# Optimization experiments

Measured on AMD Instinct MI355X. Metric: run time of the kernel, lower is better.

Reference implementation:

```python
import math
import jax, jax.numpy as jnp
import numpy as np

B = 8
NUM_POINTS = 4096
LATENT = 512
HID = 512
AD = 128
R1, R2, R_ATT = 1.0, 1.5, 0.2
EPS = 1e-5
SQRT_D = math.sqrt(AD)


def _fibonacci_sphere_points(n, radius):
    if n <= 0:
        return np.zeros((0, 3), np.float32)
    i = np.arange(n, dtype=np.float32)
    phi = (1 + 5 ** 0.5) / 2
    theta = 2 * math.pi * i / phi
    z = 1.0 - 2.0 * (i + 0.5) / n
    r_xy = np.sqrt(np.maximum(1.0 - z * z, 0.0))
    return (radius * np.stack((r_xy * np.cos(theta), r_xy * np.sin(theta), z), axis=-1)).astype(np.float32)


def _make_template():
    n_shell = NUM_POINTS - 1
    area_ratio = R1 ** 2 / (R1 ** 2 + R2 ** 2)
    n1 = max(1, round(n_shell * area_ratio))
    n2 = n_shell - n1
    if n2 == 0:
        n1, n2 = n1 - 1, 1
    t1 = _fibonacci_sphere_points(n1, R1)
    t2 = _fibonacci_sphere_points(n2, R2)
    return jnp.asarray(np.concatenate([np.zeros((1, 3), np.float32), t1, t2], axis=0))


def setup_inputs() -> dict:
    key = jax.random.key(0)
    ks = iter(jax.random.split(key, 64))
    d = {}
    d['z'] = jax.random.normal(next(ks), (B, LATENT), jnp.float32)
    d['template'] = _make_template()
    d['wq'] = jax.random.normal(next(ks), (AD, 3), jnp.float32) * 0.1
    d['wk'] = jax.random.normal(next(ks), (AD, 3), jnp.float32) * 0.1
    d['wv'] = jax.random.normal(next(ks), (AD, 3), jnp.float32) * 0.1
    in_dims = [LATENT + 3, LATENT + 3 + AD, LATENT + 3 + AD]
    for s, in_dim in enumerate(in_dims):
        d[f's{s}_w1'] = jax.random.normal(next(ks), (HID, in_dim), jnp.float32) * (1.0 / math.sqrt(in_dim))
        d[f's{s}_b1'] = jnp.zeros((HID,), jnp.float32)
        d[f's{s}_g1'] = jnp.ones((HID,), jnp.float32)
        d[f's{s}_be1'] = jnp.zeros((HID,), jnp.float32)
        d[f's{s}_w2'] = jax.random.normal(next(ks), (HID, HID), jnp.float32) * (1.0 / math.sqrt(HID))
        d[f's{s}_b2'] = jnp.zeros((HID,), jnp.float32)
        d[f's{s}_g2'] = jnp.ones((HID,), jnp.float32)
        d[f's{s}_be2'] = jnp.zeros((HID,), jnp.float32)
        d[f's{s}_w3'] = jax.random.normal(next(ks), (3, HID), jnp.float32) * (1.0 / math.sqrt(HID))
        d[f's{s}_b3'] = jnp.zeros((3,), jnp.float32)
    return d


def _bn_relu(x, gamma, beta):
    # BatchNorm1d in training mode over channel dim of (B, N, C): stats over (B, N)
    mean = jnp.mean(x, axis=(0, 1))
    var = jnp.var(x, axis=(0, 1))
    xn = (x - mean) * jax.lax.rsqrt(var + EPS)
    return jax.nn.relu(xn * gamma + beta)


def _stage(x, w1, b1, g1, be1, w2, b2, g2, be2, w3, b3):
    h = _bn_relu(x @ w1.T + b1, g1, be1)
    h = _bn_relu(h @ w2.T + b2, g2, be2)
    return h @ w3.T + b3


def _local_attention(coords, wq, wk, wv):
    Q = coords @ wq.T  # (B, N, AD)
    K = coords @ wk.T
    V = coords @ wv.T
    sq = jnp.sum(coords * coords, axis=-1)  # (B, N)
    D2 = sq[:, :, None] + sq[:, None, :] - 2.0 * jnp.einsum('bnd,bmd->bnm', coords, coords)
    mask = D2 <= R_ATT ** 2  # diagonal always True (D2=0)
    scores = jnp.einsum('bnd,bmd->bnm', Q, K) / SQRT_D
    scores = jnp.where(mask, scores, -jnp.inf)
    W = jax.nn.softmax(scores, axis=-1)
    W = jnp.where(mask, W, 0.0)
    return jnp.einsum('bnm,bmd->bnd', W, V)


def reference(z, template, wq, wk, wv,
              s0_w1, s0_b1, s0_g1, s0_be1, s0_w2, s0_b2, s0_g2, s0_be2, s0_w3, s0_b3,
              s1_w1, s1_b1, s1_g1, s1_be1, s1_w2, s1_b2, s1_g2, s1_be2, s1_w3, s1_b3,
              s2_w1, s2_b1, s2_g1, s2_be1, s2_w2, s2_b2, s2_g2, s2_be2, s2_w3, s2_b3):
    Bz = z.shape[0]
    z_exp = jnp.broadcast_to(z[:, None, :], (Bz, NUM_POINTS, LATENT))
    tmpl = jnp.broadcast_to(template[None], (Bz, NUM_POINTS, 3))
    coords0 = _stage(jnp.concatenate((z_exp, tmpl), axis=-1),
                     s0_w1, s0_b1, s0_g1, s0_be1, s0_w2, s0_b2, s0_g2, s0_be2, s0_w3, s0_b3)
    attn1 = _local_attention(coords0, wq, wk, wv)
    coords1 = _stage(jnp.concatenate((z_exp, coords0, attn1), axis=-1),
                     s1_w1, s1_b1, s1_g1, s1_be1, s1_w2, s1_b2, s1_g2, s1_be2, s1_w3, s1_b3)
    attn2 = _local_attention(coords1, wq, wk, wv)
    coords2 = _stage(jnp.concatenate((z_exp, coords1, attn2), axis=-1),
                     s2_w1, s2_b1, s2_g1, s2_be1, s2_w2, s2_b2, s2_g2, s2_be2, s2_w3, s2_b3)
    return coords2
```

## Files before the change

### kernel.cpp

```cpp
#include <hip/hip_runtime.h>
#include <math.h>

#define NPTS 4096
#define BATCH 8
#define HIDD 512
#define ROWS 32768
#define R_ATT2 0.04f
#define INV_SQRT_D 0.08838834764831845f
#define LOG2E 1.4426950408889634f

typedef unsigned short u16;
typedef unsigned int u32;
typedef __attribute__((ext_vector_type(8))) short s8v;
typedef __attribute__((ext_vector_type(4))) float f4v;
typedef __attribute__((ext_vector_type(4))) u32 u4v;
typedef __attribute__((ext_vector_type(2))) u32 u2v;

__device__ __forceinline__ float u2f(u16 v) { return __uint_as_float(((u32)v) << 16); }
__device__ __forceinline__ u16 f2u(float f) {
  u32 u = __float_as_uint(f);
  return (u16)((u + 0x7fffu + ((u >> 16) & 1u)) >> 16);
}
__device__ __forceinline__ u32 packtrunc(float x0, float x1) {
  return (__float_as_uint(x1) & 0xFFFF0000u) | (__float_as_uint(x0) >> 16);
}
__device__ __forceinline__ float fast_exp2(float x) {
  float r;
  asm("v_exp_f32 %0, %1" : "=v"(r) : "v"(x));
  return r;
}
__device__ __forceinline__ s8v mk8(u32 a, u32 b, u32 c, u32 d) {
  union { u4v u; s8v s; } x;
  x.u = (u4v){a, b, c, d};
  return x.s;
}

__global__ void gram_k(const float* __restrict__ wq, const float* __restrict__ wk,
                       float* __restrict__ G) {
  int ab = threadIdx.x;
  if (ab < 9) {
    int a = ab / 3, b = ab % 3;
    float s = 0.f;
    for (int d = 0; d < 128; ++d) s = fmaf(wq[d * 3 + a], wk[d * 3 + b], s);
    G[ab] = s;
  }
}

__global__ __launch_bounds__(256) void prep2_k(
    const float* __restrict__ z, const float* __restrict__ w1, int ldw,
    const float* __restrict__ b1, const float* __restrict__ w2,
    float* __restrict__ zwbuf, float* __restrict__ ubuf,
    u16* __restrict__ w1abf, u16* __restrict__ w2bf, int doW1a) {
  int wid = blockIdx.x * 4 + (threadIdx.x >> 6);
  int lane = threadIdx.x & 63;
  {
    int b = wid >> 9, c = wid & 511;
    const float* zr = z + b * 512;
    const float* wr = w1 + (size_t)c * ldw;
    float acc = 0.f;
#pragma unroll
    for (int k = lane; k < 512; k += 64) acc = fmaf(zr[k], wr[k], acc);
#pragma unroll
    for (int off = 32; off; off >>= 1) acc += __shfl_down(acc, off);
    if (lane == 0) zwbuf[wid] = acc + b1[c];
  }
  int idx = blockIdx.x * 256 + threadIdx.x;
  if (idx < 1536) {
    int a = idx >> 9, c = idx & 511;
    ubuf[idx] = w1[(size_t)c * ldw + 512 + a];
  }
  if (doW1a && idx < 65536) {
    int n = idx >> 7, k = idx & 127;
    w1abf[idx] = f2u(w1[(size_t)n * 643 + 515 + k]);
  }
  w2bf[idx] = f2u(w2[idx]);
}

__global__ __launch_bounds__(256) void s0l1s_k(const float* __restrict__ tmpl,
                                               const float* __restrict__ u,
                                               const float* __restrict__ zw,
                                               u16* __restrict__ h,
                                               float* __restrict__ psum,
                                               float* __restrict__ psumsq) {
  __shared__ float Ls[4][512];
  __shared__ float Lq[4][512];
  int g = blockIdx.x;
  int wave = threadIdx.x >> 6, lane = threadIdx.x & 63;
  int b = g >> 8;
  int c0 = lane * 8;
  const float* zr = zw + b * 512 + c0;
  const float* u0 = u + c0;
  const float* u1 = u + 512 + c0;
  const float* u2 = u + 1024 + c0;
  float zv[8], u0v[8], u1v[8], u2v[8];
#pragma unroll
  for (int j = 0; j < 8; ++j) {
    zv[j] = zr[j]; u0v[j] = u0[j]; u1v[j] = u1[j]; u2v[j] = u2[j];
  }
  float s[8] = {0, 0, 0, 0, 0, 0, 0, 0}, q[8] = {0, 0, 0, 0, 0, 0, 0, 0};
  int row0 = g * 16 + wave * 4;
#pragma unroll
  for (int t = 0; t < 4; ++t) {
    int row = row0 + t;
    int n = row & (NPTS - 1);
    float tx = tmpl[n * 3], ty = tmpl[n * 3 + 1], tz = tmpl[n * 3 + 2];
    u32 outw[4];
#pragma unroll
    for (int jj = 0; jj < 4; ++jj) {
      float v0 = zv[2 * jj] + tx * u0v[2 * jj] + ty * u1v[2 * jj] + tz * u2v[2 * jj];
      float v1 = zv[2 * jj + 1] + tx * u0v[2 * jj + 1] + ty * u1v[2 * jj + 1] + tz * u2v[2 * jj + 1];
      outw[jj] = packtrunc(v0, v1);
      float r0 = u2f((u16)(outw[jj] & 0xffffu));
      float r1 = u2f((u16)(outw[jj] >> 16));
      s[2 * jj] += r0;     q[2 * jj] = fmaf(r0, r0, q[2 * jj]);
      s[2 * jj + 1] += r1; q[2 * jj + 1] = fmaf(r1, r1, q[2 * jj + 1]);
    }
    *(uint4*)(h + (size_t)row * 512 + c0) = *(const uint4*)outw;
  }
#pragma unroll
  for (int j = 0; j < 8; ++j) {
    Ls[wave][c0 + j] = s[j];
    Lq[wave][c0 + j] = q[j];
  }
  __syncthreads();
  int c2 = threadIdx.x * 2;
#pragma unroll
  for (int cc = 0; cc < 2; ++cc) {
    int c = c2 + cc;
    psum[g * 512 + c] = Ls[0][c] + Ls[1][c] + Ls[2][c] + Ls[3][c];
    psumsq[g * 512 + c] = Lq[0][c] + Lq[1][c] + Lq[2][c] + Lq[3][c];
  }
}

__global__ __launch_bounds__(256) void bnrelu_k(u16* __restrict__ h,
                                                const float* __restrict__ sc,
                                                const float* __restrict__ sh) {
  int nthreads = gridDim.x * 256;
  int total = ROWS * 512 / 8;
  for (int i = blockIdx.x * 256 + threadIdx.x; i < total; i += nthreads) {
    int k0 = (i * 8) & 511;
    uint4 v = *(const uint4*)(h + (size_t)i * 8);
    const u16* p = (const u16*)&v;
    u32 outw[4];
#pragma unroll
    for (int t = 0; t < 4; ++t) {
      float x0 = fmaxf(fmaf(u2f(p[2 * t]), sc[k0 + 2 * t], sh[k0 + 2 * t]), 0.f);
      float x1 = fmaxf(fmaf(u2f(p[2 * t + 1]), sc[k0 + 2 * t + 1], sh[k0 + 2 * t + 1]), 0.f);
      outw[t] = packtrunc(x0, x1);
    }
    *(uint4*)(h + (size_t)i * 8) = *(const uint4*)outw;
  }
}

template <bool MODE1>
__global__ __launch_bounds__(256) void gemm_mfma_k(
    const u16* __restrict__ A, int lda, const u16* __restrict__ B, int ldb, int K,
    const float* __restrict__ bias, const float* __restrict__ zw,
    const float* __restrict__ u, const float4* __restrict__ c4,
    u16* __restrict__ C, float* __restrict__ psum, float* __restrict__ psumsq) {
  __shared__ u16 As[2][128 * 32];
  __shared__ u16 Bs[2][128 * 32];
  int tid = threadIdx.x;
  int wave = tid >> 6, lane = tid & 63;
  int quad = lane >> 4, l16 = lane & 15;
  int m0 = blockIdx.x * 128, n0 = blockIdx.y * 128;
  int wm = (wave & 1) * 64, wn = (wave >> 1) * 64;
  int srow0 = lane >> 2;
  int sc8 = (lane & 3) * 8;
  f4v acc[4][4];
#pragma unroll
  for (int mi = 0; mi < 4; ++mi)
#pragma unroll
    for (int ni = 0; ni < 4; ++ni) acc[mi][ni] = (f4v){0.f, 0.f, 0.f, 0.f};

  int chunk = wave * 2;
  int row0 = chunk * 16 + srow0;
  const u16* gA0 = A + (size_t)(m0 + row0) * lda + sc8;
  const u16* gA1 = A + (size_t)(m0 + row0 + 16) * lda + sc8;
  const u16* gB0 = B + (size_t)(n0 + row0) * ldb + sc8;
  const u16* gB1 = B + (size_t)(n0 + row0 + 16) * ldb + sc8;

  auto stage = [&](int nb, int k0) {
    __builtin_amdgcn_global_load_lds(
        (const __attribute__((address_space(1))) void*)(gA0 + k0),
        (__attribute__((address_space(3))) void*)(As[nb] + chunk * 512), 16, 0, 0);
    __builtin_amdgcn_global_load_lds(
        (const __attribute__((address_space(1))) void*)(gA1 + k0),
        (__attribute__((address_space(3))) void*)(As[nb] + (chunk + 1) * 512), 16, 0, 0);
    __builtin_amdgcn_global_load_lds(
        (const __attribute__((address_space(1))) void*)(gB0 + k0),
        (__attribute__((address_space(3))) void*)(Bs[nb] + chunk * 512), 16, 0, 0);
    __builtin_amdgcn_global_load_lds(
        (const __attribute__((address_space(1))) void*)(gB1 + k0),
        (__attribute__((address_space(3))) void*)(Bs[nb] + (chunk + 1) * 512), 16, 0, 0);
  };

  int NT = K >> 5;
  stage(0, 0);
  __syncthreads();
  int cur = 0;
  for (int t = 0; t < NT; ++t) {
    if (t + 1 < NT) stage(cur ^ 1, (t + 1) * 32);
    s8v af[4], bfv[4];
#pragma unroll
    for (int mi = 0; mi < 4; ++mi)
      af[mi] = *(const s8v*)&As[cur][(wm + mi * 16 + l16) * 32 + quad * 8];
#pragma unroll
    for (int ni = 0; ni < 4; ++ni)
      bfv[ni] = *(const s8v*)&Bs[cur][(wn + ni * 16 + l16) * 32 + quad * 8];
#pragma unroll
    for (int mi = 0; mi < 4; ++mi)
#pragma unroll
      for (int ni = 0; ni < 4; ++ni)
        acc[mi][ni] = __builtin_amdgcn_mfma_f32_16x16x32_bf16(
            af[mi], bfv[ni], acc[mi][ni], 0, 0, 0);
    __syncthreads();
    cur ^= 1;
  }

  int batch = m0 >> 12;
  float e0[4], e1[4], e2[4], e3[4];
  float ps[4] = {0, 0, 0, 0}, pq[4] = {0, 0, 0, 0};
#pragma unroll
  for (int ni = 0; ni < 4; ++ni) {
    int gn = n0 + wn + ni * 16 + l16;
    if (MODE1) {
      e0[ni] = zw[batch * 512 + gn];
      e1[ni] = u[gn];
      e2[ni] = u[512 + gn];
      e3[ni] = u[1024 + gn];
    } else {
      e0[ni] = bias[gn];
    }
  }
#pragma unroll
  for (int mi = 0; mi < 4; ++mi) {
#pragma unroll
    for (int reg = 0; reg < 4; ++reg) {
      int gm = m0 + wm + mi * 16 + quad * 4 + reg;
      float cx = 0.f, cy = 0.f, cz = 0.f;
      if (MODE1) {
        float4 p = c4[gm];
        cx = p.x; cy = p.y; cz = p.z;
      }
#pragma unroll
      for (int ni = 0; ni < 4; ++ni) {
        int gn = n0 + wn + ni * 16 + l16;
        float v = acc[mi][ni][reg] + e0[ni];
        if (MODE1) v += cx * e1[ni] + cy * e2[ni] + cz * e3[ni];
        u16 r = f2u(v);
        C[(size_t)gm * 512 + gn] = r;
        float vr = u2f(r);
        ps[ni] += vr;
        pq[ni] = fmaf(vr, vr, pq[ni]);
      }
    }
  }
  float* Lps = (float*)As;
  float* Lpq = (float*)Bs;
#pragma unroll
  for (int ni = 0; ni < 4; ++ni) {
    Lps[((wave * 4 + quad) * 4 + ni) * 16 + l16] = ps[ni];
    Lpq[((wave * 4 + quad) * 4 + ni) * 16 + l16] = pq[ni];
  }
  __syncthreads();
  if (tid < 128) {
    int wn2 = tid >> 6, rem = tid & 63;
    int nni = rem >> 4, ll = rem & 15;
    int gn = n0 + wn2 * 64 + nni * 16 + ll;
    float s = 0.f, q = 0.f;
#pragma unroll
    for (int wv = 0; wv < 2; ++wv)
#pragma unroll
      for (int qd = 0; qd < 4; ++qd) {
        int w2 = wn2 * 2 + wv;
        s += Lps[((w2 * 4 + qd) * 4 + nni) * 16 + ll];
        q += Lpq[((w2 * 4 + qd) * 4 + nni) * 16 + ll];
      }
    psum[(size_t)blockIdx.x * 512 + gn] = s;
    psumsq[(size_t)blockIdx.x * 512 + gn] = q;
  }
}

__global__ __launch_bounds__(256) void bn_fin_k(
    const float* __restrict__ psum, const float* __restrict__ psumsq, int nslabs,
    const float* __restrict__ gamma, const float* __restrict__ beta,
    float* __restrict__ sc, float* __restrict__ sh) {
  int c = blockIdx.x * 4 + (threadIdx.x >> 6);
  int lane = threadIdx.x & 63;
  float s = 0.f, q = 0.f;
  for (int g = lane; g < nslabs; g += 64) {
    s += psum[g * 512 + c];
    q += psumsq[g * 512 + c];
  }
#pragma unroll
  for (int off = 32; off; off >>= 1) {
    s += __shfl_down(s, off);
    q += __shfl_down(q, off);
  }
  if (lane == 0) {
    float mean = s * (1.f / 32768.f);
    float var = fmaxf(q * (1.f / 32768.f) - mean * mean, 0.f);
    float inv = rsqrtf(var + 1e-5f);
    float scale = gamma[c] * inv;
    sc[c] = scale;
    sh[c] = beta[c] - mean * scale;
  }
}

__global__ __launch_bounds__(256) void l3_k(const u16* __restrict__ h,
                                            const float* __restrict__ sc,
                                            const float* __restrict__ sh,
                                            const float* __restrict__ w3,
                                            const float* __restrict__ b3,
                                            float4* __restrict__ c4out,
                                            float* __restrict__ fout) {
  int wid = blockIdx.x * 4 + (threadIdx.x >> 6);
  int lane = threadIdx.x & 63;
  int k0 = lane * 8;
  uint4 hv = *(const uint4*)(h + (size_t)wid * 512 + k0);
  const u16* hp = (const u16*)&hv;
  float a0 = 0, a1 = 0, a2 = 0;
#pragma unroll
  for (int j = 0; j < 8; ++j) {
    int k = k0 + j;
    float x = fmaxf(fmaf(u2f(hp[j]), sc[k], sh[k]), 0.f);
    a0 = fmaf(x, w3[k], a0);
    a1 = fmaf(x, w3[512 + k], a1);
    a2 = fmaf(x, w3[1024 + k], a2);
  }
#pragma unroll
  for (int off = 32; off; off >>= 1) {
    a0 += __shfl_down(a0, off);
    a1 += __shfl_down(a1, off);
    a2 += __shfl_down(a2, off);
  }
  if (lane == 0) {
    a0 += b3[0]; a1 += b3[1]; a2 += b3[2];
    if (c4out) {
      float sq = a0 * a0 + a1 * a1 + a2 * a2;
      c4out[wid] = make_float4(a0, a1, a2, sq);
    }
    if (fout) {
      fout[(size_t)wid * 3 + 0] = a0;
      fout[(size_t)wid * 3 + 1] = a1;
      fout[(size_t)wid * 3 + 2] = a2;
    }
  }
}

__global__ __launch_bounds__(256) void cprep_k(const float4* __restrict__ c4,
                                               u4v* __restrict__ frag,
                                               u16* __restrict__ ctg) {
  int i = blockIdx.x * 256 + threadIdx.x;
  float4 p = c4[i];
  float nhw = -0.5f * p.w;
  u16 hx = f2u(p.x), hy = f2u(p.y), hz = f2u(p.z), hw = f2u(nhw);
  u16 lx = f2u(p.x - u2f(hx)), ly = f2u(p.y - u2f(hy));
  u16 lz = f2u(p.z - u2f(hz)), lw = f2u(nhw - u2f(hw));
  u32 h01 = (u32)hx | ((u32)hy << 16), h23 = (u32)hz | ((u32)hw << 16);
  u32 l01 = (u32)lx | ((u32)ly << 16), l23 = (u32)lz | ((u32)lw << 16);
  frag[i] = (u4v){h01, h23, l01, l23};
  int chunk = i >> 5, p32 = i & 31;
  u16* base = ctg + (size_t)chunk * 128;
  base[p32] = 0x3F80;
  base[32 + p32] = hx;
  base[64 + p32] = hy;
  base[96 + p32] = hz;
}

__global__ __launch_bounds__(512) void attnm_k(const float4* __restrict__ c4,
                                               const u4v* __restrict__ frag,
                                               const u16* __restrict__ ctg,
                                               const float* __restrict__ G,
                                               const float* __restrict__ wv,
                                               u16* __restrict__ attnb) {
  __shared__ __align__(16) char lds[20480 + 4096];
  int wave = threadIdx.x >> 6, lane = threadIdx.x & 63;
  int g = lane >> 4, q16 = lane & 15;
  int qbase = blockIdx.x * 32;
  int b = qbase >> 12;
  int pt0 = wave * 512;
  char* ebuf = lds + wave * 2560;
  float* fin = (float*)(lds + 20480);
  int chunk0 = b * 128 + (pt0 >> 5);

  float Gr[9];
#pragma unroll
  for (int i = 0; i < 9; ++i) Gr[i] = G[i];
  u32 bh0[2], bh1[2], bh2[2], bh3[2];
  u32 sh0[2], sh1[2], sh2[2], sh3[2];
  float thr[2];
#pragma unroll
  for (int s = 0; s < 2; ++s) {
    float4 cq = c4[qbase + s * 16 + q16];
    thr[s] = 0.5f * (cq.w - R_ATT2);
    u16 hx = f2u(cq.x), hy = f2u(cq.y), hz = f2u(cq.z);
    u16 lx = f2u(cq.x - u2f(hx)), ly = f2u(cq.y - u2f(hy)), lz = f2u(cq.z - u2f(hz));
    u32 h01 = (u32)hx | ((u32)hy << 16);
    u32 h23 = (u32)hz | (0x3F80u << 16);
    u32 l01 = (u32)lx | ((u32)ly << 16);
    u32 l23 = (u32)lz;
    bh0[s] = (g <= 1) ? h01 : 0u;
    bh1[s] = (g <= 1) ? h23 : 0u;
    bh2[s] = (g == 0) ? l01 : 0u;
    bh3[s] = (g == 0) ? l23 : 0u;
    const float SC = INV_SQRT_D * LOG2E;
    float g0v = (cq.x * Gr[0] + cq.y * Gr[3] + cq.z * Gr[6]) * SC;
    float g1v = (cq.x * Gr[1] + cq.y * Gr[4] + cq.z * Gr[7]) * SC;
    float g2v = (cq.x * Gr[2] + cq.y * Gr[5] + cq.z * Gr[8]) * SC;
    u16 ghx = f2u(g0v), ghy = f2u(g1v), ghz = f2u(g2v);
    u16 glx = f2u(g0v - u2f(ghx)), gly = f2u(g1v - u2f(ghy)), glz = f2u(g2v - u2f(ghz));
    u32 gh01 = (u32)ghx | ((u32)ghy << 16);
    u32 gh23 = (u32)ghz;
    u32 gl01 = (u32)glx | ((u32)gly << 16);
    u32 gl23 = (u32)glz;
    sh0[s] = (g <= 1) ? gh01 : 0u;
    sh1[s] = (g <= 1) ? gh23 : 0u;
    sh2[s] = (g == 0) ? gl01 : 0u;
    sh3[s] = (g == 0) ? gl23 : 0u;
  }

  f4v pvAcc[2];
#pragma unroll
  for (int s = 0; s < 2; ++s) pvAcc[s] = (f4v){0.f, 0.f, 0.f, 0.f};

  int csw = g ^ (q16 & 3);
  for (int w = 0; w < 16; ++w) {
#pragma unroll
    for (int tp = 0; tp < 2; ++tp) {
      int p = pt0 + w * 32 + tp * 16 + q16;
      u4v f = frag[(size_t)b * NPTS + p];
      u32 a0 = (g == 0) ? f.x : ((g == 1) ? f.z : 0u);
      u32 a1 = (g == 0) ? f.y : ((g == 1) ? f.w : 0u);
      u32 a2 = (g == 0) ? f.x : 0u;
      u32 a3 = (g == 0) ? f.y : 0u;
      s8v av = mk8(a0, a1, a2, a3);
      int wsw = ((tp * 2 + (g >> 1)) ^ (q16 & 3)) * 16 + (g & 1) * 8;
#pragma unroll
      for (int s = 0; s < 2; ++s) {
        f4v z4 = (f4v){0.f, 0.f, 0.f, 0.f};
        f4v dmv = __builtin_amdgcn_mfma_f32_16x16x32_bf16(
            av, mk8(bh0[s], bh1[s], bh2[s], bh3[s]), z4, 0, 0, 0);
        f4v s2v = __builtin_amdgcn_mfma_f32_16x16x32_bf16(
            av, mk8(sh0[s], sh1[s], sh2[s], sh3[s]), z4, 0, 0, 0);
        float e0 = (dmv[0] >= thr[s]) ? fast_exp2(s2v[0]) : 0.f;
        float e1 = (dmv[1] >= thr[s]) ? fast_exp2(s2v[1]) : 0.f;
        float e2 = (dmv[2] >= thr[s]) ? fast_exp2(s2v[2]) : 0.f;
        float e3 = (dmv[3] >= thr[s]) ? fast_exp2(s2v[3]) : 0.f;
        u2v ew = (u2v){packtrunc(e0, e1), packtrunc(e2, e3)};
        *(u2v*)(ebuf + s * 1280 + q16 * 80 + wsw) = ew;
      }
    }
    const u16* ctb = ctg + (size_t)(chunk0 + w) * 128 + (q16 & 3) * 32 + g * 8;
    u4v bt = *(const u4v*)ctb;
    s8v pvB = mk8(bt.x, bt.y, bt.z, bt.w);
#pragma unroll
    for (int s = 0; s < 2; ++s) {
      u4v at = *(const u4v*)(ebuf + s * 1280 + q16 * 80 + csw * 16);
      pvAcc[s] = __builtin_amdgcn_mfma_f32_16x16x32_bf16(
          mk8(at.x, at.y, at.z, at.w), pvB, pvAcc[s], 0, 0, 0);
    }
  }

  if (q16 < 4) {
#pragma unroll
    for (int s = 0; s < 2; ++s)
#pragma unroll
      for (int r = 0; r < 4; ++r)
        fin[wave * 128 + (s * 16 + g * 4 + r) * 4 + q16] = pvAcc[s][r];
  }
  __syncthreads();
  float* comb = (float*)lds;
  int t = threadIdx.x;
  if (t < 128) {
    int qb = t >> 2, c = t & 3;
    float acc = 0.f;
#pragma unroll
    for (int wv8 = 0; wv8 < 8; ++wv8) acc += fin[wv8 * 128 + qb * 4 + c];
    comb[qb * 4 + c] = acc;
  }
  __syncthreads();
#pragma unroll
  for (int it = 0; it < 4; ++it) {
    int task = t + it * 512;
    int qb = task >> 6, dp = task & 63;
    float sw = comb[qb * 4 + 0];
    float sx = comb[qb * 4 + 1];
    float sy = comb[qb * 4 + 2];
    float sz = comb[qb * 4 + 3];
    float inv = 1.f / sw;
    float ox = sx * inv, oy = sy * inv, oz = sz * inv;
    int d0 = dp * 2;
    float v0 = ox * wv[d0 * 3] + oy * wv[d0 * 3 + 1] + oz * wv[d0 * 3 + 2];
    float v1 = ox * wv[d0 * 3 + 3] + oy * wv[d0 * 3 + 4] + oz * wv[d0 * 3 + 5];
    u32 pack = (u32)f2u(v0) | ((u32)f2u(v1) << 16);
    *(u32*)(attnb + (size_t)(qbase + qb) * 128 + d0) = pack;
  }
}

extern "C" void kernel_launch(void* const* d_in, const int* in_sizes, int n_in,
                              void* d_out, int out_size, void* d_ws, size_t ws_size,
                              hipStream_t stream) {
  const float* z = (const float*)d_in[0];
  const float* tmpl = (const float*)d_in[1];
  const float* wq = (const float*)d_in[2];
  const float* wk = (const float*)d_in[3];
  const float* wv = (const float*)d_in[4];
  const float* sw[3][10];
  for (int s = 0; s < 3; ++s)
    for (int j = 0; j < 10; ++j) sw[s][j] = (const float*)d_in[5 + s * 10 + j];

  char* base = (char*)d_ws;
  size_t off = 0;
  auto alloc = [&](size_t bytes) -> void* {
    void* p = base + off;
    off = (off + bytes + 255) & ~(size_t)255;
    return p;
  };
  u16* hA = (u16*)alloc((size_t)ROWS * 512 * 2);
  u16* hB = (u16*)alloc((size_t)ROWS * 512 * 2);
  u16* attnb = (u16*)alloc((size_t)ROWS * 128 * 2);
  float4* c4 = (float4*)alloc((size_t)ROWS * 16);
  float* psum = (float*)alloc(2048 * 512 * 4);
  float* psumsq = (float*)alloc(2048 * 512 * 4);
  float* zwbuf = (float*)alloc(4096 * 4);
  float* scv = (float*)alloc(512 * 4);
  float* shv = (float*)alloc(512 * 4);
  float* G = (float*)alloc(256);
  u16* w1abf = (u16*)alloc(512 * 128 * 2);
  u16* w2bf = (u16*)alloc(512 * 512 * 2);
  float* ubuf = (float*)alloc(1536 * 4);
  u4v* fragb = (u4v*)alloc((size_t)ROWS * 16);
  u16* ctg = (u16*)alloc((size_t)1024 * 128 * 2);

  gram_k<<<1, 64, 0, stream>>>(wq, wk, G);

  for (int s = 0; s < 3; ++s) {
    int ldw = (s == 0) ? 515 : 643;
    prep2_k<<<1024, 256, 0, stream>>>(z, sw[s][0], ldw, sw[s][1], sw[s][4],
                                      zwbuf, ubuf, w1abf, w2bf, s == 0 ? 0 : 1);
    if (s == 0) {
      s0l1s_k<<<2048, 256, 0, stream>>>(tmpl, ubuf, zwbuf, hA, psum, psumsq);
      bn_fin_k<<<128, 256, 0, stream>>>(psum, psumsq, 2048,
                                        sw[s][2], sw[s][3], scv, shv);
    } else {
      gemm_mfma_k<true><<<dim3(256, 4), 256, 0, stream>>>(
          attnb, 128, w1abf, 128, 128, nullptr, zwbuf, ubuf, c4,
          hA, psum, psumsq);
      bn_fin_k<<<128, 256, 0, stream>>>(psum, psumsq, 256,
                                        sw[s][2], sw[s][3], scv, shv);
    }
    bnrelu_k<<<2048, 256, 0, stream>>>(hA, scv, shv);
    gemm_mfma_k<false><<<dim3(256, 4), 256, 0, stream>>>(
        hA, 512, w2bf, 512, 512, sw[s][5], nullptr, nullptr, nullptr,
        hB, psum, psumsq);
    bn_fin_k<<<128, 256, 0, stream>>>(psum, psumsq, 256,
                                      sw[s][6], sw[s][7], scv, shv);
    bool last = (s == 2);
    l3_k<<<8192, 256, 0, stream>>>(hB, scv, shv, sw[s][8], sw[s][9],
                                   last ? nullptr : c4,
                                   last ? (float*)d_out : nullptr);
    if (!last) {
      cprep_k<<<128, 256, 0, stream>>>(c4, fragb, ctg);
      attnm_k<<<1024, 512, 0, stream>>>(c4, fragb, ctg, G, wv, attnb);
    }
  }
}
```

Measured before the change: 464.5 us.

## Fuse BN finalize into consumers via atomic stats and fold cprep into l3

The GEMM epilogues now reduce their per-channel batch-norm sums straight into 512-entry buffers with atomicAdd, and the zeroing happens in prep2_k. The separate bn_fin_k launches are removed, and each consumer (bnrelu_k, l3_k) recomputes scale and shift from the raw sums, gamma and beta. The cprep fragment packing moves into the l3_k epilogue. Together this drops several small kernel launches and a pass over the coordinates, in exchange for atomic contention and fp32 atomic summation order that is no longer deterministic.

```diff
diff --git a/kernel.cpp b/kernel.cpp
--- a/kernel.cpp
+++ b/kernel.cpp
@@ -33,6 +33,14 @@
   union { u4v u; s8v s; } x;
   x.u = (u4v){a, b, c, d};
   return x.s;
+}
+__device__ __forceinline__ void bn_coef(float s, float q, float gam, float bet,
+                                        float& sc, float& sh) {
+  float mean = s * (1.f / 32768.f);
+  float var = fmaxf(q * (1.f / 32768.f) - mean * mean, 0.f);
+  float inv = rsqrtf(var + 1e-5f);
+  sc = gam * inv;
+  sh = bet - mean * sc;
 }
 
 __global__ void gram_k(const float* __restrict__ wq, const float* __restrict__ wk,
@@ -50,7 +58,9 @@
     const float* __restrict__ z, const float* __restrict__ w1, int ldw,
     const float* __restrict__ b1, const float* __restrict__ w2,
     float* __restrict__ zwbuf, float* __restrict__ ubuf,
-    u16* __restrict__ w1abf, u16* __restrict__ w2bf, int doW1a) {
+    u16* __restrict__ w1abf, u16* __restrict__ w2bf, int doW1a,
+    float* __restrict__ psA, float* __restrict__ pqA,
+    float* __restrict__ psB, float* __restrict__ pqB) {
   int wid = blockIdx.x * 4 + (threadIdx.x >> 6);
   int lane = threadIdx.x & 63;
   {
@@ -68,6 +78,10 @@
   if (idx < 1536) {
     int a = idx >> 9, c = idx & 511;
     ubuf[idx] = w1[(size_t)c * ldw + 512 + a];
+  }
+  if (idx < 512) {
+    psA[idx] = 0.f; pqA[idx] = 0.f;
+    psB[idx] = 0.f; pqB[idx] = 0.f;
   }
   if (doW1a && idx < 65536) {
     int n = idx >> 7, k = idx & 127;
@@ -132,20 +146,48 @@
   }
 }
 
+__global__ __launch_bounds__(256) void bn_red_k(
+    const float* __restrict__ psum, const float* __restrict__ psumsq,
+    float* __restrict__ psA, float* __restrict__ pqA) {
+  int c = blockIdx.x * 4 + (threadIdx.x >> 6);
+  int lane = threadIdx.x & 63;
+  float s = 0.f, q = 0.f;
+  for (int g = lane; g < 2048; g += 64) {
+    s += psum[g * 512 + c];
+    q += psumsq[g * 512 + c];
+  }
+#pragma unroll
+  for (int off = 32; off; off >>= 1) {
+    s += __shfl_down(s, off);
+    q += __shfl_down(q, off);
+  }
+  if (lane == 0) {
+    psA[c] = s;
+    pqA[c] = q;
+  }
+}
+
 __global__ __launch_bounds__(256) void bnrelu_k(u16* __restrict__ h,
-                                                const float* __restrict__ sc,
-                                                const float* __restrict__ sh) {
+                                                const float* __restrict__ ps,
+                                                const float* __restrict__ pq,
+                                                const float* __restrict__ gamma,
+                                                const float* __restrict__ beta) {
+  int i0 = blockIdx.x * 256 + threadIdx.x;
+  int k0 = (i0 * 8) & 511;
+  float scv[8], shv[8];
+#pragma unroll
+  for (int j = 0; j < 8; ++j)
+    bn_coef(ps[k0 + j], pq[k0 + j], gamma[k0 + j], beta[k0 + j], scv[j], shv[j]);
   int nthreads = gridDim.x * 256;
   int total = ROWS * 512 / 8;
-  for (int i = blockIdx.x * 256 + threadIdx.x; i < total; i += nthreads) {
-    int k0 = (i * 8) & 511;
+  for (int i = i0; i < total; i += nthreads) {
     uint4 v = *(const uint4*)(h + (size_t)i * 8);
     const u16* p = (const u16*)&v;
     u32 outw[4];
 #pragma unroll
     for (int t = 0; t < 4; ++t) {
-      float x0 = fmaxf(fmaf(u2f(p[2 * t]), sc[k0 + 2 * t], sh[k0 + 2 * t]), 0.f);
-      float x1 = fmaxf(fmaf(u2f(p[2 * t + 1]), sc[k0 + 2 * t + 1], sh[k0 + 2 * t + 1]), 0.f);
+      float x0 = fmaxf(fmaf(u2f(p[2 * t]), scv[2 * t], shv[2 * t]), 0.f);
+      float x1 = fmaxf(fmaf(u2f(p[2 * t + 1]), scv[2 * t + 1], shv[2 * t + 1]), 0.f);
       outw[t] = packtrunc(x0, x1);
     }
     *(uint4*)(h + (size_t)i * 8) = *(const uint4*)outw;
@@ -277,57 +319,38 @@
         s += Lps[((w2 * 4 + qd) * 4 + nni) * 16 + ll];
         q += Lpq[((w2 * 4 + qd) * 4 + nni) * 16 + ll];
       }
-    psum[(size_t)blockIdx.x * 512 + gn] = s;
-    psumsq[(size_t)blockIdx.x * 512 + gn] = q;
-  }
-}
-
-__global__ __launch_bounds__(256) void bn_fin_k(
-    const float* __restrict__ psum, const float* __restrict__ psumsq, int nslabs,
-    const float* __restrict__ gamma, const float* __restrict__ beta,
-    float* __restrict__ sc, float* __restrict__ sh) {
-  int c = blockIdx.x * 4 + (threadIdx.x >> 6);
-  int lane = threadIdx.x & 63;
-  float s = 0.f, q = 0.f;
-  for (int g = lane; g < nslabs; g += 64) {
-    s += psum[g * 512 + c];
-    q += psumsq[g * 512 + c];
-  }
-#pragma unroll
-  for (int off = 32; off; off >>= 1) {
-    s += __shfl_down(s, off);
-    q += __shfl_down(q, off);
-  }
-  if (lane == 0) {
-    float mean = s * (1.f / 32768.f);
-    float var = fmaxf(q * (1.f / 32768.f) - mean * mean, 0.f);
-    float inv = rsqrtf(var + 1e-5f);
-    float scale = gamma[c] * inv;
-    sc[c] = scale;
-    sh[c] = beta[c] - mean * scale;
+    atomicAdd(&psum[gn], s);
+    atomicAdd(&psumsq[gn], q);
   }
 }
 
 __global__ __launch_bounds__(256) void l3_k(const u16* __restrict__ h,
-                                            const float* __restrict__ sc,
-                                            const float* __restrict__ sh,
+                                            const float* __restrict__ ps,
+                                            const float* __restrict__ pq,
+                                            const float* __restrict__ gamma,
+                                            const float* __restrict__ beta,
                                             const float* __restrict__ w3,
                                             const float* __restrict__ b3,
                                             float4* __restrict__ c4out,
-                                            float* __restrict__ fout) {
+                                            float* __restrict__ fout,
+                                            u4v* __restrict__ frag,
+                                            u16* __restrict__ ctg) {
   int wid = blockIdx.x * 4 + (threadIdx.x >> 6);
   int lane = threadIdx.x & 63;
   int k0 = lane * 8;
+  float scv[8], shv[8];
+#pragma unroll
+  for (int j = 0; j < 8; ++j)
+    bn_coef(ps[k0 + j], pq[k0 + j], gamma[k0 + j], beta[k0 + j], scv[j], shv[j]);
   uint4 hv = *(const uint4*)(h + (size_t)wid * 512 + k0);
   const u16* hp = (const u16*)&hv;
   float a0 = 0, a1 = 0, a2 = 0;
 #pragma unroll
   for (int j = 0; j < 8; ++j) {
-    int k = k0 + j;
-    float x = fmaxf(fmaf(u2f(hp[j]), sc[k], sh[k]), 0.f);
-    a0 = fmaf(x, w3[k], a0);
-    a1 = fmaf(x, w3[512 + k], a1);
-    a2 = fmaf(x, w3[1024 + k], a2);
+    float x = fmaxf(fmaf(u2f(hp[j]), scv[j], shv[j]), 0.f);
+    a0 = fmaf(x, w3[k0 + j], a0);
+    a1 = fmaf(x, w3[512 + k0 + j], a1);
+    a2 = fmaf(x, w3[1024 + k0 + j], a2);
   }
 #pragma unroll
   for (int off = 32; off; off >>= 1) {
@@ -340,6 +363,19 @@
     if (c4out) {
       float sq = a0 * a0 + a1 * a1 + a2 * a2;
       c4out[wid] = make_float4(a0, a1, a2, sq);
+      float nhw = -0.5f * sq;
+      u16 hx = f2u(a0), hy = f2u(a1), hz = f2u(a2), hw = f2u(nhw);
+      u16 lx = f2u(a0 - u2f(hx)), ly = f2u(a1 - u2f(hy));
+      u16 lz = f2u(a2 - u2f(hz)), lw = f2u(nhw - u2f(hw));
+      u32 h01 = (u32)hx | ((u32)hy << 16), h23 = (u32)hz | ((u32)hw << 16);
+      u32 l01 = (u32)lx | ((u32)ly << 16), l23 = (u32)lz | ((u32)lw << 16);
+      frag[wid] = (u4v){h01, h23, l01, l23};
+      int chunk = wid >> 5, p32 = wid & 31;
+      u16* basep = ctg + (size_t)chunk * 128;
+      basep[p32] = 0x3F80;
+      basep[32 + p32] = hx;
+      basep[64 + p32] = hy;
+      basep[96 + p32] = hz;
     }
     if (fout) {
       fout[(size_t)wid * 3 + 0] = a0;
@@ -347,26 +383,6 @@
       fout[(size_t)wid * 3 + 2] = a2;
     }
   }
-}
-
-__global__ __launch_bounds__(256) void cprep_k(const float4* __restrict__ c4,
-                                               u4v* __restrict__ frag,
-                                               u16* __restrict__ ctg) {
-  int i = blockIdx.x * 256 + threadIdx.x;
-  float4 p = c4[i];
-  float nhw = -0.5f * p.w;
-  u16 hx = f2u(p.x), hy = f2u(p.y), hz = f2u(p.z), hw = f2u(nhw);
-  u16 lx = f2u(p.x - u2f(hx)), ly = f2u(p.y - u2f(hy));
-  u16 lz = f2u(p.z - u2f(hz)), lw = f2u(nhw - u2f(hw));
-  u32 h01 = (u32)hx | ((u32)hy << 16), h23 = (u32)hz | ((u32)hw << 16);
-  u32 l01 = (u32)lx | ((u32)ly << 16), l23 = (u32)lz | ((u32)lw << 16);
-  frag[i] = (u4v){h01, h23, l01, l23};
-  int chunk = i >> 5, p32 = i & 31;
-  u16* base = ctg + (size_t)chunk * 128;
-  base[p32] = 0x3F80;
-  base[32 + p32] = hx;
-  base[64 + p32] = hy;
-  base[96 + p32] = hz;
 }
 
 __global__ __launch_bounds__(512) void attnm_k(const float4* __restrict__ c4,
@@ -525,8 +541,10 @@
   float* psum = (float*)alloc(2048 * 512 * 4);
   float* psumsq = (float*)alloc(2048 * 512 * 4);
   float* zwbuf = (float*)alloc(4096 * 4);
-  float* scv = (float*)alloc(512 * 4);
-  float* shv = (float*)alloc(512 * 4);
+  float* psA = (float*)alloc(512 * 4);
+  float* pqA = (float*)alloc(512 * 4);
+  float* psB = (float*)alloc(512 * 4);
+  float* pqB = (float*)alloc(512 * 4);
   float* G = (float*)alloc(256);
   u16* w1abf = (u16*)alloc(512 * 128 * 2);
   u16* w2bf = (u16*)alloc(512 * 512 * 2);
@@ -539,30 +557,27 @@
   for (int s = 0; s < 3; ++s) {
     int ldw = (s == 0) ? 515 : 643;
     prep2_k<<<1024, 256, 0, stream>>>(z, sw[s][0], ldw, sw[s][1], sw[s][4],
-                                      zwbuf, ubuf, w1abf, w2bf, s == 0 ? 0 : 1);
+                                      zwbuf, ubuf, w1abf, w2bf, s == 0 ? 0 : 1,
+                                      psA, pqA, psB, pqB);
     if (s == 0) {
       s0l1s_k<<<2048, 256, 0, stream>>>(tmpl, ubuf, zwbuf, hA, psum, psumsq);
-      bn_fin_k<<<128, 256, 0, stream>>>(psum, psumsq, 2048,
-                                        sw[s][2], sw[s][3], scv, shv);
+      bn_red_k<<<128, 256, 0, stream>>>(psum, psumsq, psA, pqA);
     } else {
       gemm_mfma_k<true><<<dim3(256, 4), 256, 0, stream>>>(
           attnb, 128, w1abf, 128, 128, nullptr, zwbuf, ubuf, c4,
-          hA, psum, psumsq);
-      bn_fin_k<<<128, 256, 0, stream>>>(psum, psumsq, 256,
-                                        sw[s][2], sw[s][3], scv, shv);
-    }
-    bnrelu_k<<<2048, 256, 0, stream>>>(hA, scv, shv);
+          hA, psA, pqA);
+    }
+    bnrelu_k<<<2048, 256, 0, stream>>>(hA, psA, pqA, sw[s][2], sw[s][3]);
     gemm_mfma_k<false><<<dim3(256, 4), 256, 0, stream>>>(
         hA, 512, w2bf, 512, 512, sw[s][5], nullptr, nullptr, nullptr,
-        hB, psum, psumsq);
-    bn_fin_k<<<128, 256, 0, stream>>>(psum, psumsq, 256,
-                                      sw[s][6], sw[s][7], scv, shv);
+        hB, psB, pqB);
     bool last = (s == 2);
-    l3_k<<<8192, 256, 0, stream>>>(hB, scv, shv, sw[s][8], sw[s][9],
+    l3_k<<<8192, 256, 0, stream>>>(hB, psB, pqB, sw[s][6], sw[s][7],
+                                   sw[s][8], sw[s][9],
                                    last ? nullptr : c4,
-                                   last ? (float*)d_out : nullptr);
+                                   last ? (float*)d_out : nullptr,
+                                   fragb, ctg);
     if (!last) {
-      cprep_k<<<128, 256, 0, stream>>>(c4, fragb, ctg);
       attnm_k<<<1024, 512, 0, stream>>>(c4, fragb, ctg, G, wv, attnb);
     }
   }
```

Measured after the change: 497.1 us. 7.0% more time.
